# Performance work log

Measured on AMD Instinct MI355X. Metric: run time of the kernel, lower is better.

The kernel has to match this reference:

```python
import jax, jax.numpy as jnp
import numpy as np

B, T, D, W, H = 4096, 1, 4096, 4, 512  # batch, step len, hidden, kernel_size, generator hidden


def setup_inputs() -> dict:
    key = jax.random.key(0)
    ks = jax.random.split(key, 5)
    x = jax.random.normal(ks[0], (B, T, D), dtype=jnp.float32)
    generator_input = jax.random.normal(ks[1], (B, T, D), dtype=jnp.float32)
    cache = jax.random.normal(ks[2], (B, D, W), dtype=jnp.float32)
    w1 = jax.random.normal(ks[3], (D, H), dtype=jnp.float32) * 0.02
    w2 = jax.random.normal(ks[4], (H, D * W), dtype=jnp.float32) * 0.02
    b2 = jnp.zeros((D * W,), dtype=jnp.float32)
    return {"x": x, "generator_input": generator_input, "cache": cache,
            "w1": w1, "w2": w2, "b2": b2}


def reference(x, generator_input, cache, w1, w2, b2):
    # --- kernel generator (DynamicShortConvolutionKernelGenerator) ---
    g = generator_input[:, 0]                        # [B, D]  (squeeze(1) in _step_triton)
    h = jax.nn.silu(g @ w1)                          # [B, H]
    flat_kernels = h @ w2 + b2                       # [B, D*W]
    kernels = flat_kernels.reshape(B, D, W)          # [B, D, W]  (rearrange 'b (d w) -> b d w')
    # --- causal_conv_step_triton: shift window left, append new token ---
    x_t = jnp.swapaxes(x, 1, 2)                      # [B, D, 1]
    new_cache = jnp.concatenate([cache[:, :, 1:], x_t], axis=-1)  # [B, D, W]
    # depthwise dynamic conv: per-token, per-channel kernel dot window
    out = jnp.sum(new_cache * kernels, axis=-1)      # [B, D]
    out = jax.nn.silu(out)[:, None, :]               # [B, 1, D] (view back to x shape)
    return out, new_cache
```

## Files before the change

### kernel.cpp

```cpp
#include <hip/hip_runtime.h>
#include <hip/hip_bf16.h>
#include <math.h>

#define B_  4096
#define D_  4096
#define W_  4
#define H_  512
#define NDW (D_*W_)

typedef float  f32x4  __attribute__((ext_vector_type(4)));
typedef __bf16 bf16x8 __attribute__((ext_vector_type(8)));

__device__ __forceinline__ unsigned short f32_to_bf16(float f) {
    unsigned int u = __float_as_uint(f);
    u += 0x7fffu + ((u >> 16) & 1u);
    return (unsigned short)(u >> 16);
}

__device__ __forceinline__ float silu_f(float v) {
    return v / (1.0f + __expf(-v));
}

__global__ void cast_g_kernel(const float* __restrict__ in,
                              unsigned short* __restrict__ out, int n4) {
    int i = blockIdx.x * blockDim.x + threadIdx.x;
    if (i >= n4) return;
    float4 v = ((const float4*)in)[i];
    ushort4 o;
    o.x = f32_to_bf16(v.x); o.y = f32_to_bf16(v.y);
    o.z = f32_to_bf16(v.z); o.w = f32_to_bf16(v.w);
    ((ushort4*)out)[i] = o;
}

__global__ void transpose_cast_kernel(const float* __restrict__ in,
                                      unsigned short* __restrict__ out,
                                      int R, int C) {
    __shared__ unsigned short tile[64][65];
    const int r0 = blockIdx.y * 64;
    const int c0 = blockIdx.x * 64;
    const int tx = threadIdx.x & 63;
    const int ty = threadIdx.x >> 6;
#pragma unroll
    for (int rr = ty; rr < 64; rr += 4)
        tile[rr][tx] = f32_to_bf16(in[(size_t)(r0 + rr) * C + c0 + tx]);
    __syncthreads();
#pragma unroll
    for (int cc = ty; cc < 64; cc += 4)
        out[(size_t)(c0 + cc) * R + r0 + tx] = tile[tx][cc];
}

__global__ __launch_bounds__(256)
void gemm1_silu(const unsigned short* __restrict__ A,
                const unsigned short* __restrict__ Bt,
                unsigned short* __restrict__ Hout,
                int M, int N, int K)
{
    __shared__ unsigned short As[64 * 64];
    __shared__ unsigned short Bs[128 * 64];

    const int tid  = threadIdx.x;
    const int wave = tid >> 6;
    const int lane = tid & 63;
    const int quad = lane >> 4;
    const int l16  = lane & 15;
    const int m0 = blockIdx.y * 64;
    const int n0 = blockIdx.x * 128;
    const int wm = (wave >> 1) * 32;
    const int wn = (wave & 1) * 64;

    f32x4 acc[2][4];
#pragma unroll
    for (int i = 0; i < 2; ++i)
#pragma unroll
        for (int j = 0; j < 4; ++j)
            acc[i][j] = (f32x4){0.f, 0.f, 0.f, 0.f};

    for (int k0 = 0; k0 < K; k0 += 64) {
#pragma unroll
        for (int r = 0; r < 2; ++r) {
            const int flat  = r * 256 + tid;
            const int row   = flat >> 3;
            const int chunk = flat & 7;
            const unsigned short* gA = A + (size_t)(m0 + row) * K + (k0 + chunk * 8);
            unsigned short* lA = As + (size_t)(r * 256 + wave * 64) * 8;
            __builtin_amdgcn_global_load_lds(
                (const __attribute__((address_space(1))) void*)gA,
                (__attribute__((address_space(3))) void*)lA, 16, 0, 0);
        }
#pragma unroll
        for (int r = 0; r < 4; ++r) {
            const int flat  = r * 256 + tid;
            const int row   = flat >> 3;
            const int chunk = flat & 7;
            const unsigned short* gB = Bt + (size_t)(n0 + row) * K + (k0 + chunk * 8);
            unsigned short* lB = Bs + (size_t)(r * 256 + wave * 64) * 8;
            __builtin_amdgcn_global_load_lds(
                (const __attribute__((address_space(1))) void*)gB,
                (__attribute__((address_space(3))) void*)lB, 16, 0, 0);
        }
        __syncthreads();

#pragma unroll
        for (int ks = 0; ks < 2; ++ks) {
            const int kk = ks * 32 + quad * 8;
            bf16x8 af[2], bfr[4];
#pragma unroll
            for (int i = 0; i < 2; ++i)
                af[i]  = *(const bf16x8*)(As + (wm + i * 16 + l16) * 64 + kk);
#pragma unroll
            for (int j = 0; j < 4; ++j)
                bfr[j] = *(const bf16x8*)(Bs + (wn + j * 16 + l16) * 64 + kk);
#pragma unroll
            for (int i = 0; i < 2; ++i)
#pragma unroll
                for (int j = 0; j < 4; ++j)
                    acc[i][j] = __builtin_amdgcn_mfma_f32_16x16x32_bf16(
                        af[i], bfr[j], acc[i][j], 0, 0, 0);
        }
        __syncthreads();
    }

#pragma unroll
    for (int i = 0; i < 2; ++i)
#pragma unroll
        for (int j = 0; j < 4; ++j) {
            const int col = n0 + wn + j * 16 + l16;
#pragma unroll
            for (int r = 0; r < 4; ++r) {
                const int row = m0 + wm + i * 16 + quad * 4 + r;
                Hout[(size_t)row * N + col] = f32_to_bf16(silu_f(acc[i][j][r]));
            }
        }
}

__global__ __launch_bounds__(256)
void gemm2_conv(const unsigned short* __restrict__ A,
                const unsigned short* __restrict__ Bt,
                const float* __restrict__ bias,
                const float* __restrict__ x,
                const float* __restrict__ cache,
                float* __restrict__ out,
                float* __restrict__ ncache)
{
    __shared__ __align__(16) unsigned short smem[128 * 68 * 2];
    unsigned short* As = smem;
    unsigned short* Bs = smem + 128 * 64;
    float* Cs = (float*)smem;

    const int tid  = threadIdx.x;
    const int wave = tid >> 6;
    const int lane = tid & 63;
    const int quad = lane >> 4;
    const int l16  = lane & 15;
    const int m0 = blockIdx.y * 128;
    const int n0 = blockIdx.x * 128;
    const int wm = (wave >> 1) * 64;
    const int wn = (wave & 1) * 64;
    const int K = H_;

    f32x4 acc[4][4];
#pragma unroll
    for (int i = 0; i < 4; ++i)
#pragma unroll
        for (int j = 0; j < 4; ++j)
            acc[i][j] = (f32x4){0.f, 0.f, 0.f, 0.f};

    for (int k0 = 0; k0 < K; k0 += 64) {
#pragma unroll
        for (int r = 0; r < 4; ++r) {
            const int flat  = r * 256 + tid;
            const int row   = flat >> 3;
            const int chunk = flat & 7;
            const unsigned short* gA = A  + (size_t)(m0 + row) * K + (k0 + chunk * 8);
            const unsigned short* gB = Bt + (size_t)(n0 + row) * K + (k0 + chunk * 8);
            unsigned short* lA = As + (size_t)(r * 256 + wave * 64) * 8;
            unsigned short* lB = Bs + (size_t)(r * 256 + wave * 64) * 8;
            __builtin_amdgcn_global_load_lds(
                (const __attribute__((address_space(1))) void*)gA,
                (__attribute__((address_space(3))) void*)lA, 16, 0, 0);
            __builtin_amdgcn_global_load_lds(
                (const __attribute__((address_space(1))) void*)gB,
                (__attribute__((address_space(3))) void*)lB, 16, 0, 0);
        }
        __syncthreads();

#pragma unroll
        for (int ks = 0; ks < 2; ++ks) {
            const int kk = ks * 32 + quad * 8;
            bf16x8 af[4], bfr[4];
#pragma unroll
            for (int i = 0; i < 4; ++i) {
                af[i]  = *(const bf16x8*)(As + (wm + i * 16 + l16) * 64 + kk);
                bfr[i] = *(const bf16x8*)(Bs + (wn + i * 16 + l16) * 64 + kk);
            }
#pragma unroll
            for (int i = 0; i < 4; ++i)
#pragma unroll
                for (int j = 0; j < 4; ++j)
                    acc[i][j] = __builtin_amdgcn_mfma_f32_16x16x32_bf16(
                        af[i], bfr[j], acc[i][j], 0, 0, 0);
        }
        __syncthreads();
    }

#pragma unroll
    for (int h = 0; h < 2; ++h) {
        if ((wave & 1) == h) {
#pragma unroll
            for (int i = 0; i < 4; ++i)
#pragma unroll
                for (int j = 0; j < 4; ++j) {
                    const int lc = j * 16 + l16;
                    const float bv = bias[n0 + h * 64 + lc];
#pragma unroll
                    for (int r = 0; r < 4; ++r) {
                        const int lr = wm + i * 16 + quad * 4 + r;
                        Cs[lr * 68 + lc] = acc[i][j][r] + bv;
                    }
                }
        }
        __syncthreads();

        const int dp    = tid & 15;
        const int rbase = tid >> 4;
        const int d     = (n0 >> 2) + h * 16 + dp;
#pragma unroll
        for (int rr = 0; rr < 8; ++rr) {
            const int br = rr * 16 + rbase;
            const size_t gi = (size_t)(m0 + br) * D_ + d;
            f32x4 k4 = *(const f32x4*)(Cs + br * 68 + dp * 4);
            f32x4 c4 = ((const f32x4*)cache)[gi];
            float xv = x[gi];
            f32x4 nc = { c4.y, c4.z, c4.w, xv };
            float s = nc.x * k4.x + nc.y * k4.y + nc.z * k4.z + nc.w * k4.w;
            out[gi] = silu_f(s);
            ((f32x4*)ncache)[gi] = nc;
        }
        __syncthreads();
    }
}

extern "C" void kernel_launch(void* const* d_in, const int* in_sizes, int n_in,
                              void* d_out, int out_size, void* d_ws, size_t ws_size,
                              hipStream_t stream) {
    const float* x     = (const float*)d_in[0];
    const float* gin   = (const float*)d_in[1];
    const float* cache = (const float*)d_in[2];
    const float* w1    = (const float*)d_in[3];
    const float* w2    = (const float*)d_in[4];
    const float* b2    = (const float*)d_in[5];

    float* out    = (float*)d_out;
    float* ncache = out + (size_t)B_ * D_;

    unsigned short* g_bf = (unsigned short*)d_ws;
    unsigned short* w1t  = g_bf + (size_t)B_ * D_;
    unsigned short* w2t  = w1t + (size_t)H_ * D_;
    unsigned short* h_bf = w2t + (size_t)NDW * H_;

    cast_g_kernel<<<(B_ * D_ / 4 + 255) / 256, 256, 0, stream>>>(gin, g_bf, B_ * D_ / 4);
    transpose_cast_kernel<<<dim3(H_ / 64, D_ / 64), 256, 0, stream>>>(w1, w1t, D_, H_);
    transpose_cast_kernel<<<dim3(NDW / 64, H_ / 64), 256, 0, stream>>>(w2, w2t, H_, NDW);

    gemm1_silu<<<dim3(H_ / 128, B_ / 64), 256, 0, stream>>>(
        g_bf, w1t, h_bf, B_, H_, D_);

    gemm2_conv<<<dim3(NDW / 128, B_ / 128), 256, 0, stream>>>(
        h_bf, w2t, b2, x, cache, out, ncache);
}
```

Before: 776.8 us.

## Double-buffer and swizzle LDS in both GEMMs, fuse conv epilogue via DPP

Both GEMMs now double-buffer their LDS tiles so the next tile's global-to-LDS load overlaps the current tile's MFMA work, and use an XOR swizzle on LDS chunks to avoid bank conflicts. GEMM1 drops to a 64x64 tile to launch more blocks, and GEMM2 remaps block indices for better L2 locality. The conv epilogue skips the LDS staging round-trip: each lane reads one window element, and the 4-tap sum is reduced across lanes with DPP moves. In exchange the epilogue issues scalar strided global loads and stores in place of 16-byte vector ones, and the larger LDS footprint may limit occupancy.

Measured after the change: 1.009 ms. 29.9% more time.

```diff
diff --git a/kernel.cpp b/kernel.cpp
--- a/kernel.cpp
+++ b/kernel.cpp
@@ -19,6 +19,13 @@
 
 __device__ __forceinline__ float silu_f(float v) {
     return v / (1.0f + __expf(-v));
+}
+
+__device__ __forceinline__ float qxor1(float v) {
+    return __int_as_float(__builtin_amdgcn_mov_dpp(__float_as_int(v), 0xB1, 0xF, 0xF, true));
+}
+__device__ __forceinline__ float qxor2(float v) {
+    return __int_as_float(__builtin_amdgcn_mov_dpp(__float_as_int(v), 0x4E, 0xF, 0xF, true));
 }
 
 __global__ void cast_g_kernel(const float* __restrict__ in,
@@ -49,14 +56,12 @@
         out[(size_t)(c0 + cc) * R + r0 + tx] = tile[tx][cc];
 }
 
-__global__ __launch_bounds__(256)
+__global__ __launch_bounds__(256, 2)
 void gemm1_silu(const unsigned short* __restrict__ A,
                 const unsigned short* __restrict__ Bt,
-                unsigned short* __restrict__ Hout,
-                int M, int N, int K)
+                unsigned short* __restrict__ Hout)
 {
-    __shared__ unsigned short As[64 * 64];
-    __shared__ unsigned short Bs[128 * 64];
+    __shared__ __align__(16) unsigned short smem[16384];
 
     const int tid  = threadIdx.x;
     const int wave = tid >> 6;
@@ -64,76 +69,88 @@
     const int quad = lane >> 4;
     const int l16  = lane & 15;
     const int m0 = blockIdx.y * 64;
-    const int n0 = blockIdx.x * 128;
+    const int n0 = blockIdx.x * 64;
     const int wm = (wave >> 1) * 32;
-    const int wn = (wave & 1) * 64;
-
-    f32x4 acc[2][4];
+    const int wn = (wave & 1) * 32;
+
+    f32x4 acc[2][2];
 #pragma unroll
     for (int i = 0; i < 2; ++i)
 #pragma unroll
-        for (int j = 0; j < 4; ++j)
+        for (int j = 0; j < 2; ++j)
             acc[i][j] = (f32x4){0.f, 0.f, 0.f, 0.f};
 
-    for (int k0 = 0; k0 < K; k0 += 64) {
-#pragma unroll
-        for (int r = 0; r < 2; ++r) {
-            const int flat  = r * 256 + tid;
-            const int row   = flat >> 3;
-            const int chunk = flat & 7;
-            const unsigned short* gA = A + (size_t)(m0 + row) * K + (k0 + chunk * 8);
-            unsigned short* lA = As + (size_t)(r * 256 + wave * 64) * 8;
-            __builtin_amdgcn_global_load_lds(
-                (const __attribute__((address_space(1))) void*)gA,
-                (__attribute__((address_space(3))) void*)lA, 16, 0, 0);
-        }
-#pragma unroll
-        for (int r = 0; r < 4; ++r) {
-            const int flat  = r * 256 + tid;
-            const int row   = flat >> 3;
-            const int chunk = flat & 7;
-            const unsigned short* gB = Bt + (size_t)(n0 + row) * K + (k0 + chunk * 8);
-            unsigned short* lB = Bs + (size_t)(r * 256 + wave * 64) * 8;
-            __builtin_amdgcn_global_load_lds(
-                (const __attribute__((address_space(1))) void*)gB,
-                (__attribute__((address_space(3))) void*)lB, 16, 0, 0);
-        }
+#define STAGE1(bufOff, k0)                                                          \
+    {                                                                               \
+        _Pragma("unroll")                                                           \
+        for (int r_ = 0; r_ < 2; ++r_) {                                            \
+            const int flat_ = r_ * 256 + tid;                                       \
+            const int row_  = flat_ >> 3;                                           \
+            const int ch_   = (flat_ & 7) ^ (row_ & 7);    \
+            const unsigned short* gA_ = A  + (size_t)(m0 + row_) * D_ + (k0) + ch_ * 8; \
+            const unsigned short* gB_ = Bt + (size_t)(n0 + row_) * D_ + (k0) + ch_ * 8; \
+            unsigned short* lA_ = smem + (bufOff) + (r_ * 256 + wave * 64) * 8;     \
+            unsigned short* lB_ = smem + (bufOff) + 4096 + (r_ * 256 + wave * 64) * 8; \
+            __builtin_amdgcn_global_load_lds(                                       \
+                (const __attribute__((address_space(1))) void*)gA_,                 \
+                (__attribute__((address_space(3))) void*)lA_, 16, 0, 0);            \
+            __builtin_amdgcn_global_load_lds(                                       \
+                (const __attribute__((address_space(1))) void*)gB_,                 \
+                (__attribute__((address_space(3))) void*)lB_, 16, 0, 0);            \
+        }                                                                           \
+    }
+
+#define COMP1(bufOff)                                                               \
+    {                                                                               \
+        const unsigned short* cA_ = smem + (bufOff);                                \
+        const unsigned short* cB_ = smem + (bufOff) + 4096;                         \
+        _Pragma("unroll")                                                           \
+        for (int ks_ = 0; ks_ < 2; ++ks_) {                                         \
+            const int sl_ = ks_ * 4 + quad;                                         \
+            bf16x8 af_[2], bf_[2];                                                  \
+            _Pragma("unroll")                                                       \
+            for (int i_ = 0; i_ < 2; ++i_) {                                        \
+                const int ra_ = wm + i_ * 16 + l16;                                 \
+                const int rb_ = wn + i_ * 16 + l16;                                 \
+                af_[i_] = *(const bf16x8*)(cA_ + ra_ * 64 + ((sl_ ^ (ra_ & 7)) * 8)); \
+                bf_[i_] = *(const bf16x8*)(cB_ + rb_ * 64 + ((sl_ ^ (rb_ & 7)) * 8)); \
+            }                                                                       \
+            _Pragma("unroll")                                                       \
+            for (int i_ = 0; i_ < 2; ++i_)                                          \
+                _Pragma("unroll")                                                   \
+                for (int j_ = 0; j_ < 2; ++j_)                                      \
+                    acc[i_][j_] = __builtin_amdgcn_mfma_f32_16x16x32_bf16(          \
+                        af_[i_], bf_[j_], acc[i_][j_], 0, 0, 0);                    \
+        }                                                                           \
+    }
+
+    STAGE1(0, 0);
+    __syncthreads();
+    for (int t = 0; t < 63; ++t) {
+        const int cur = (t & 1) * 8192;
+        const int nxt = 8192 - cur;
+        STAGE1(nxt, (t + 1) * 64);
+        COMP1(cur);
         __syncthreads();
-
-#pragma unroll
-        for (int ks = 0; ks < 2; ++ks) {
-            const int kk = ks * 32 + quad * 8;
-            bf16x8 af[2], bfr[4];
-#pragma unroll
-            for (int i = 0; i < 2; ++i)
-                af[i]  = *(const bf16x8*)(As + (wm + i * 16 + l16) * 64 + kk);
-#pragma unroll
-            for (int j = 0; j < 4; ++j)
-                bfr[j] = *(const bf16x8*)(Bs + (wn + j * 16 + l16) * 64 + kk);
-#pragma unroll
-            for (int i = 0; i < 2; ++i)
-#pragma unroll
-                for (int j = 0; j < 4; ++j)
-                    acc[i][j] = __builtin_amdgcn_mfma_f32_16x16x32_bf16(
-                        af[i], bfr[j], acc[i][j], 0, 0, 0);
-        }
-        __syncthreads();
-    }
+    }
+    COMP1(8192);
 
 #pragma unroll
     for (int i = 0; i < 2; ++i)
 #pragma unroll
-        for (int j = 0; j < 4; ++j) {
+        for (int j = 0; j < 2; ++j) {
             const int col = n0 + wn + j * 16 + l16;
 #pragma unroll
             for (int r = 0; r < 4; ++r) {
                 const int row = m0 + wm + i * 16 + quad * 4 + r;
-                Hout[(size_t)row * N + col] = f32_to_bf16(silu_f(acc[i][j][r]));
+                Hout[(size_t)row * H_ + col] = f32_to_bf16(silu_f(acc[i][j][r]));
             }
         }
-}
-
-__global__ __launch_bounds__(256)
+#undef STAGE1
+#undef COMP1
+}
+
+__global__ __launch_bounds__(256, 2)
 void gemm2_conv(const unsigned short* __restrict__ A,
                 const unsigned short* __restrict__ Bt,
                 const float* __restrict__ bias,
@@ -142,21 +159,21 @@
                 float* __restrict__ out,
                 float* __restrict__ ncache)
 {
-    __shared__ __align__(16) unsigned short smem[128 * 68 * 2];
-    unsigned short* As = smem;
-    unsigned short* Bs = smem + 128 * 64;
-    float* Cs = (float*)smem;
+    __shared__ __align__(16) unsigned short smem[32768];
 
     const int tid  = threadIdx.x;
     const int wave = tid >> 6;
     const int lane = tid & 63;
     const int quad = lane >> 4;
     const int l16  = lane & 15;
-    const int m0 = blockIdx.y * 128;
-    const int n0 = blockIdx.x * 128;
+
+    const int bid = blockIdx.y * gridDim.x + blockIdx.x;
+    const int swz = (bid & 7) * 512 + (bid >> 3);
+    const int m0 = (swz & 31) * 128;
+    const int n0 = (swz >> 5) * 128;
+
     const int wm = (wave >> 1) * 64;
     const int wn = (wave & 1) * 64;
-    const int K = H_;
 
     f32x4 acc[4][4];
 #pragma unroll
@@ -165,78 +182,86 @@
         for (int j = 0; j < 4; ++j)
             acc[i][j] = (f32x4){0.f, 0.f, 0.f, 0.f};
 
-    for (int k0 = 0; k0 < K; k0 += 64) {
-#pragma unroll
-        for (int r = 0; r < 4; ++r) {
-            const int flat  = r * 256 + tid;
-            const int row   = flat >> 3;
-            const int chunk = flat & 7;
-            const unsigned short* gA = A  + (size_t)(m0 + row) * K + (k0 + chunk * 8);
-            const unsigned short* gB = Bt + (size_t)(n0 + row) * K + (k0 + chunk * 8);
-            unsigned short* lA = As + (size_t)(r * 256 + wave * 64) * 8;
-            unsigned short* lB = Bs + (size_t)(r * 256 + wave * 64) * 8;
-            __builtin_amdgcn_global_load_lds(
-                (const __attribute__((address_space(1))) void*)gA,
-                (__attribute__((address_space(3))) void*)lA, 16, 0, 0);
-            __builtin_amdgcn_global_load_lds(
-                (const __attribute__((address_space(1))) void*)gB,
-                (__attribute__((address_space(3))) void*)lB, 16, 0, 0);
+#define STAGE2(bufOff, k0)                                                          \
+    {                                                                               \
+        _Pragma("unroll")                                                           \
+        for (int r_ = 0; r_ < 4; ++r_) {                                            \
+            const int flat_ = r_ * 256 + tid;                                       \
+            const int row_  = flat_ >> 3;                                           \
+            const int ch_   = (flat_ & 7) ^ (row_ & 7);    \
+            const unsigned short* gA_ = A  + (size_t)(m0 + row_) * H_ + (k0) + ch_ * 8; \
+            const unsigned short* gB_ = Bt + (size_t)(n0 + row_) * H_ + (k0) + ch_ * 8; \
+            unsigned short* lA_ = smem + (bufOff) + (r_ * 256 + wave * 64) * 8;     \
+            unsigned short* lB_ = smem + (bufOff) + 8192 + (r_ * 256 + wave * 64) * 8; \
+            __builtin_amdgcn_global_load_lds(                                       \
+                (const __attribute__((address_space(1))) void*)gA_,                 \
+                (__attribute__((address_space(3))) void*)lA_, 16, 0, 0);            \
+            __builtin_amdgcn_global_load_lds(                                       \
+                (const __attribute__((address_space(1))) void*)gB_,                 \
+                (__attribute__((address_space(3))) void*)lB_, 16, 0, 0);            \
+        }                                                                           \
+    }
+
+#define COMP2(bufOff)                                                               \
+    {                                                                               \
+        const unsigned short* cA_ = smem + (bufOff);                                \
+        const unsigned short* cB_ = smem + (bufOff) + 8192;                         \
+        _Pragma("unroll")                                                           \
+        for (int ks_ = 0; ks_ < 2; ++ks_) {                                         \
+            const int sl_ = ks_ * 4 + quad;                                         \
+            bf16x8 af_[4], bf_[4];                                                  \
+            _Pragma("unroll")                                                       \
+            for (int i_ = 0; i_ < 4; ++i_) {                                        \
+                const int ra_ = wm + i_ * 16 + l16;                                 \
+                const int rb_ = wn + i_ * 16 + l16;                                 \
+                af_[i_] = *(const bf16x8*)(cA_ + ra_ * 64 + ((sl_ ^ (ra_ & 7)) * 8)); \
+                bf_[i_] = *(const bf16x8*)(cB_ + rb_ * 64 + ((sl_ ^ (rb_ & 7)) * 8)); \
+            }                                                                       \
+            _Pragma("unroll")                                                       \
+            for (int i_ = 0; i_ < 4; ++i_)                                          \
+                _Pragma("unroll")                                                   \
+                for (int j_ = 0; j_ < 4; ++j_)                                      \
+                    acc[i_][j_] = __builtin_amdgcn_mfma_f32_16x16x32_bf16(          \
+                        af_[i_], bf_[j_], acc[i_][j_], 0, 0, 0);                    \
+        }                                                                           \
+    }
+
+    STAGE2(0, 0);
+    __syncthreads();
+#pragma unroll
+    for (int t = 0; t < 7; ++t) {
+        const int cur = (t & 1) * 16384;
+        const int nxt = 16384 - cur;
+        STAGE2(nxt, (t + 1) * 64);
+        COMP2(cur);
+        __syncthreads();
+    }
+    COMP2(16384);
+#undef STAGE2
+#undef COMP2
+
+    const int w = l16 & 3;
+#pragma unroll
+    for (int j = 0; j < 4; ++j) {
+        const int col = n0 + wn + j * 16 + l16;
+        const float bv = bias[col];
+        const int d = col >> 2;
+#pragma unroll
+        for (int i = 0; i < 4; ++i) {
+#pragma unroll
+            for (int r = 0; r < 4; ++r) {
+                const int b = m0 + wm + i * 16 + quad * 4 + r;
+                const size_t gi = (size_t)b * D_ + d;
+                const float* src = (w < 3) ? (cache + gi * 4 + w + 1) : (x + gi);
+                const float nc = *src;
+                const float kv = acc[i][j][r] + bv;
+                float p = nc * kv;
+                p += qxor1(p);
+                p += qxor2(p);
+                ncache[gi * 4 + w] = nc;
+                if (w == 0) out[gi] = silu_f(p);
+            }
         }
-        __syncthreads();
-
-#pragma unroll
-        for (int ks = 0; ks < 2; ++ks) {
-            const int kk = ks * 32 + quad * 8;
-            bf16x8 af[4], bfr[4];
-#pragma unroll
-            for (int i = 0; i < 4; ++i) {
-                af[i]  = *(const bf16x8*)(As + (wm + i * 16 + l16) * 64 + kk);
-                bfr[i] = *(const bf16x8*)(Bs + (wn + i * 16 + l16) * 64 + kk);
-            }
-#pragma unroll
-            for (int i = 0; i < 4; ++i)
-#pragma unroll
-                for (int j = 0; j < 4; ++j)
-                    acc[i][j] = __builtin_amdgcn_mfma_f32_16x16x32_bf16(
-                        af[i], bfr[j], acc[i][j], 0, 0, 0);
-        }
-        __syncthreads();
-    }
-
-#pragma unroll
-    for (int h = 0; h < 2; ++h) {
-        if ((wave & 1) == h) {
-#pragma unroll
-            for (int i = 0; i < 4; ++i)
-#pragma unroll
-                for (int j = 0; j < 4; ++j) {
-                    const int lc = j * 16 + l16;
-                    const float bv = bias[n0 + h * 64 + lc];
-#pragma unroll
-                    for (int r = 0; r < 4; ++r) {
-                        const int lr = wm + i * 16 + quad * 4 + r;
-                        Cs[lr * 68 + lc] = acc[i][j][r] + bv;
-                    }
-                }
-        }
-        __syncthreads();
-
-        const int dp    = tid & 15;
-        const int rbase = tid >> 4;
-        const int d     = (n0 >> 2) + h * 16 + dp;
-#pragma unroll
-        for (int rr = 0; rr < 8; ++rr) {
-            const int br = rr * 16 + rbase;
-            const size_t gi = (size_t)(m0 + br) * D_ + d;
-            f32x4 k4 = *(const f32x4*)(Cs + br * 68 + dp * 4);
-            f32x4 c4 = ((const f32x4*)cache)[gi];
-            float xv = x[gi];
-            f32x4 nc = { c4.y, c4.z, c4.w, xv };
-            float s = nc.x * k4.x + nc.y * k4.y + nc.z * k4.z + nc.w * k4.w;
-            out[gi] = silu_f(s);
-            ((f32x4*)ncache)[gi] = nc;
-        }
-        __syncthreads();
     }
 }
 
@@ -262,8 +287,7 @@
     transpose_cast_kernel<<<dim3(H_ / 64, D_ / 64), 256, 0, stream>>>(w1, w1t, D_, H_);
     transpose_cast_kernel<<<dim3(NDW / 64, H_ / 64), 256, 0, stream>>>(w2, w2t, H_, NDW);
 
-    gemm1_silu<<<dim3(H_ / 128, B_ / 64), 256, 0, stream>>>(
-        g_bf, w1t, h_bf, B_, H_, D_);
+    gemm1_silu<<<dim3(H_ / 64, B_ / 64), 256, 0, stream>>>(g_bf, w1t, h_bf);
 
     gemm2_conv<<<dim3(NDW / 128, B_ / 128), 256, 0, stream>>>(
         h_bf, w2t, b2, x, cache, out, ncache);
```
